# Kernel tuning notes

Hardware: AMD Instinct MI355X
Metric: run time of the kernel (lower is better)

## Reference

```python
import jax, jax.numpy as jnp
import numpy as np
import math

EPS_BN1 = 1e-3   # batch_norm1 eps
EPS_BNP = 1e-5   # predictor BN default eps


def conv1d(x, w, b=None, stride=1, padding=0, dilation=1):
    # x: (B, Cin, T), w: (Cout, Cin, K)
    out = jax.lax.conv_general_dilated(
        x, w, window_strides=(stride,), padding=[(padding, padding)],
        rhs_dilation=(dilation,), dimension_numbers=('NCH', 'OIH', 'NCH'))
    if b is not None:
        out = out + b[None, :, None]
    return out


def bn_eval(x, g, b, m, v, eps):
    scale = g / jnp.sqrt(v + eps)
    return (x - m[None, :, None]) * scale[None, :, None] + b[None, :, None]


def setup_inputs() -> dict:
    key = jax.random.key(0)
    ks = jax.random.split(key, 16)
    B, Cin, T = 16, 256, 4096
    Cout, P = 256, 32
    f32 = jnp.float32

    def n(k, shape, s):
        return s * jax.random.normal(k, shape, dtype=f32)

    inp = {
        'x': n(ks[0], (B, Cin, T), 1.0),
        'conv1_w': n(ks[1], (2 * Cout, Cin, 1), 0.06),
        'bn1_g': 1.0 + n(ks[2], (2 * Cout,), 0.1),
        'bn1_b': n(ks[3], (2 * Cout,), 0.1),
        'bn1_m': n(ks[4], (2 * Cout,), 0.1),
        'bn1_v': 1.0 + 0.1 * jax.random.uniform(ks[5], (2 * Cout,), dtype=f32),
        'conv1x1_w': n(ks[6], (1, Cin, 1), 0.06),
        'p0_w': n(ks[7], (P, 2, 31), 0.1),
        'p0_b': n(ks[8], (P,), 0.05),
        'p0bn_g': jnp.ones((P,), f32), 'p0bn_b': jnp.zeros((P,), f32),
        'p0bn_m': n(ks[9], (P,), 0.1),
        'p0bn_v': 1.0 + 0.1 * jax.random.uniform(ks[10], (P,), dtype=f32),
        'p1_w': n(ks[11], (P, P, 15), 0.05),
        'p1_b': n(ks[12], (P,), 0.05),
        'p1bn_g': jnp.ones((P,), f32), 'p1bn_b': jnp.zeros((P,), f32),
        'p1bn_m': n(ks[13], (P,), 0.1),
        'p1bn_v': 1.0 + 0.1 * jax.random.uniform(ks[14], (P,), dtype=f32),
        # last predictor conv: weight scaled by 0.01, bias = -log(2) (per __init__)
        'p2_w': 0.01 * n(ks[15], (2, P, 15), 0.05),
        'p2_b': jnp.array([-math.log(2.0), -math.log(2.0)], dtype=f32),
        'norm_mean': jnp.ones((1,), f32),  # registered buffer, eval renorm
    }
    return inp


def _forward(x, conv1_w, bn1_g, bn1_b, bn1_m, bn1_v, conv1x1_w,
             p0_w, p0_b, p0bn_g, p0bn_b, p0bn_m, p0bn_v,
             p1_w, p1_b, p1bn_g, p1bn_b, p1bn_m, p1bn_v,
             p2_w, p2_b, norm_mean):
    B, Cin, T = x.shape
    sg = jax.lax.stop_gradient

    # conv1 -> BN -> GLU(dim=1); dropout is identity in eval
    feat = bn_eval(conv1d(x, conv1_w), bn1_g, bn1_b, bn1_m, bn1_v, EPS_BN1)
    a, g = jnp.split(feat, 2, axis=1)
    feat = a * jax.nn.sigmoid(g)                     # (B, Cout, T)

    # predictor on [__x, __x^2]
    xx = conv1d(x, conv1x1_w)                        # (B, 1, T)
    h = jnp.concatenate([xx, xx * xx], axis=1)       # (B, 2, T)
    h = jax.nn.silu(bn_eval(conv1d(h, p0_w, p0_b, padding=15),
                            p0bn_g, p0bn_b, p0bn_m, p0bn_v, EPS_BNP))
    h = jax.nn.silu(bn_eval(conv1d(h, p1_w, p1_b, padding=7),
                            p1bn_g, p1bn_b, p1bn_m, p1bn_v, EPS_BNP))
    jumps = conv1d(h, p2_w, p2_b, padding=7)         # (B, 2, T)

    weights = jax.nn.sigmoid(jumps[:, 0, :])         # (B, T)
    moves = jax.nn.sigmoid(jumps[:, 1, :]) * norm_mean[0]  # eval: renorm = norm_mean
    row_renorm = jnp.maximum(jnp.mean(moves, axis=1), 1.0)
    moves = moves / row_renorm[:, None]

    features = jnp.transpose(feat, (0, 2, 1))        # (B, T, C)
    fw = features * weights[:, :, None]

    # big_pool: poses value = cumsum(moves); grad path = local window of 21 moves
    # (the k=1..20 shift loop adds grad-only terms). Window sum via cumsum diff.
    c = jnp.cumsum(moves, axis=1)
    win = c - jnp.pad(c, ((0, 0), (21, 0)))[:, :T]   # sum of moves[i-20..i]
    poses = sg(c) + win - sg(win)                    # (B, T)

    floors = jnp.floor(poses)
    ceils = floors + 1.0
    w1 = 1.0 - (poses - floors)                      # func = line: 1 - t
    w2 = 1.0 - (ceils - poses)

    # moves <= 1 (sigmoid * norm_mean=1 / row_renorm>=1) => ceils.max()+1 <= T+2
    L = T + 2                                        # static bound for out length
    C = features.shape[2]
    bidx = jnp.arange(B)[:, None]
    fi = floors.astype(jnp.int32)
    ci = fi + 1
    out = jnp.zeros((B, L, C), dtype=features.dtype)
    out = out.at[bidx, fi].add(w1[:, :, None] * fw)
    out = out.at[bidx, ci].add(w2[:, :, None] * fw)

    x_evs = jnp.transpose(out, (0, 2, 1))            # (B, C, L)
    pad = 15 - (L % 15)                              # F.pad(0, 15 - L % 15)
    return jnp.pad(x_evs, ((0, 0), (0, 0), (0, pad)))


def reference(x, conv1_w, bn1_g, bn1_b, bn1_m, bn1_v, conv1x1_w,
              p0_w, p0_b, p0bn_g, p0bn_b, p0bn_m, p0bn_v,
              p1_w, p1_b, p1bn_g, p1bn_b, p1bn_m, p1bn_v,
              p2_w, p2_b, norm_mean):
    return _forward(x, conv1_w, bn1_g, bn1_b, bn1_m, bn1_v, conv1x1_w,
                    p0_w, p0_b, p0bn_g, p0bn_b, p0bn_m, p0bn_v,
                    p1_w, p1_b, p1bn_g, p1bn_b, p1bn_m, p1bn_v,
                    p2_w, p2_b, norm_mean)
```

## Files before the change

kernel.cpp:

```cpp
#include <hip/hip_runtime.h>
#include <hip/hip_bf16.h>

#define BB   16
#define CIN  256
#define TN   4096
#define LOUT 4110
#define FTS  4224

typedef __attribute__((ext_vector_type(8))) short s16x8;
typedef __attribute__((ext_vector_type(4))) float f32x4;


__global__ __launch_bounds__(256) void k0_prep(
    const float* __restrict__ conv1_w, const float* __restrict__ p0_w,
    const float* __restrict__ p1_w, const float* __restrict__ p2_w,
    const float* __restrict__ bn1_g, const float* __restrict__ bn1_b,
    const float* __restrict__ bn1_m, const float* __restrict__ bn1_v,
    const float* __restrict__ p0_b, const float* __restrict__ p0g,
    const float* __restrict__ p0bb, const float* __restrict__ p0m,
    const float* __restrict__ p0v,
    const float* __restrict__ p1_b, const float* __restrict__ p1g,
    const float* __restrict__ p1bb, const float* __restrict__ p1m,
    const float* __restrict__ p1v,
    short* __restrict__ wBpk, float4* __restrict__ bnp,
    float* __restrict__ wp0T, short* __restrict__ wp1M,
    short* __restrict__ wp2M, float2* __restrict__ bnp0,
    float2* __restrict__ bnp1) {
  int bid = blockIdx.x, tid = threadIdx.x;
  if (bid < 512) {
    int e = bid * 256 + tid;
    int i = e & 7, l = (e >> 3) & 63, ks = (e >> 9) & 7, n16 = e >> 12;
    int n = n16 * 16 + (l & 15);
    int j = n & 63;
    int co = (j < 32) ? ((n >> 6) * 32 + j) : (256 + (n >> 6) * 32 + (j - 32));
    int ci = ks * 32 + (l >> 4) * 8 + i;
    __hip_bfloat16 hv = __float2bfloat16(conv1_w[co * 256 + ci]);
    wBpk[e] = *(short*)&hv;
  } else {
    int idx = (bid - 512) * 256 + tid;
    if (idx < 1984) {
      int ch = idx & 31, rem = idx >> 5;
      int ic = rem / 31, k = rem % 31;
      wp0T[idx] = p0_w[(ch * 2 + ic) * 31 + k];
    }
    {
      int i = idx & 7, l = (idx >> 3) & 63, nf = (idx >> 9) & 1, koff = idx >> 10;
      int ch = nf * 16 + (l & 15), ic = (l >> 4) * 8 + i;
      __hip_bfloat16 hv = __float2bfloat16(p1_w[(ch * 32 + ic) * 15 + koff]);
      wp1M[idx] = *(short*)&hv;
    }
    if (idx < 7680) {
      int i = idx & 7, l = (idx >> 3) & 63, koff = idx >> 9;
      int n = l & 15, ic = (l >> 4) * 8 + i;
      float v = (n < 2) ? p2_w[(n * 32 + ic) * 15 + koff] : 0.f;
      __hip_bfloat16 hv = __float2bfloat16(v);
      wp2M[idx] = *(short*)&hv;
    }
    if (idx < 32) {
      int ch = idx;
      float sc = p0g[ch] * rsqrtf(p0v[ch] + 1e-5f);
      bnp0[ch] = make_float2(sc, (p0_b[ch] - p0m[ch]) * sc + p0bb[ch]);
    }
    if (idx >= 32 && idx < 64) {
      int ch = idx - 32;
      float sc = p1g[ch] * rsqrtf(p1v[ch] + 1e-5f);
      bnp1[ch] = make_float2(sc, (p1_b[ch] - p1m[ch]) * sc + p1bb[ch]);
    }
    if (idx < 256) {
      int c = idx;
      float sa = bn1_g[c] * rsqrtf(bn1_v[c] + 1e-3f);
      float ba = bn1_b[c] - bn1_m[c] * sa;
      float sg = bn1_g[c + 256] * rsqrtf(bn1_v[c + 256] + 1e-3f);
      float bg = bn1_b[c + 256] - bn1_m[c + 256] * sg;
      bnp[c] = make_float4(sa, ba, sg, bg);
    }
  }
}

__global__ __launch_bounds__(256) void k0b_tr(
    const float* __restrict__ x, const float* __restrict__ w1x1,
    short* __restrict__ xT, float* __restrict__ xx) {
  int t0 = blockIdx.x * 64;
  int b = blockIdx.y;
  __shared__ float ls[64][129];
  int tid = threadIdx.x;
  const float* xb = x + (size_t)b * (CIN * TN);
  float xacc = 0.f;
  for (int half = 0; half < 2; ++half) {
    if (half) __syncthreads();
#pragma unroll
    for (int s = 0; s < 8; ++s) {
      int idx = tid + s * 256;
      int ci = idx >> 4, tc = idx & 15;
      float4 v = *(const float4*)(xb + (size_t)(half * 128 + ci) * TN + t0 + tc * 4);
      ls[tc * 4 + 0][ci] = v.x;
      ls[tc * 4 + 1][ci] = v.y;
      ls[tc * 4 + 2][ci] = v.z;
      ls[tc * 4 + 3][ci] = v.w;
    }
    __syncthreads();
    if (tid < 64) {
#pragma unroll 4
      for (int k = 0; k < 128; ++k)
        xacc = fmaf(ls[tid][k], w1x1[half * 128 + k], xacc);
    }
#pragma unroll
    for (int s = 0; s < 4; ++s) {
      int o = tid + s * 256;
      int ci8 = o & 15, t = o >> 4;
      s16x8 pk;
#pragma unroll
      for (int i = 0; i < 8; ++i) {
        __hip_bfloat16 hv = __float2bfloat16(ls[t][ci8 * 8 + i]);
        pk[i] = *(short*)&hv;
      }
      *(s16x8*)(xT + ((size_t)(b * TN) + t0 + t) * 256 + half * 128 + ci8 * 8) = pk;
    }
  }
  if (tid < 64) xx[b * TN + t0 + tid] = xacc;
}

__global__ __launch_bounds__(512) void k1_mfma(
    const short* __restrict__ xT, const short* __restrict__ wBpk,
    const float4* __restrict__ bnp, __hip_bfloat16* __restrict__ featT) {
  int ty = blockIdx.x, b = blockIdx.y;
  int t0 = ty * 64;
  __shared__ __align__(16) short As[64 * 256];
  int tid = threadIdx.x;
  int l = tid & 63, wv = tid >> 6;
  const short* xb = xT + ((size_t)b * TN + t0) * 256;

#pragma unroll
  for (int it = 0; it < 4; ++it) {
    int r = it * 16 + wv * 2 + (l >> 5);
    int gs = (l & 31) ^ (r & 7);
    const short* gp = xb + r * 256 + gs * 8;
    __builtin_amdgcn_global_load_lds(
        (const __attribute__((address_space(1))) void*)gp,
        (__attribute__((address_space(3))) void*)(As + (it * 16 + wv * 2) * 256),
        16, 0, 0);
  }
  __syncthreads();

  f32x4 acc[4][4];
#pragma unroll
  for (int i = 0; i < 4; ++i)
#pragma unroll
    for (int j = 0; j < 4; ++j) acc[i][j] = (f32x4){0.f, 0.f, 0.f, 0.f};

  int lr = l & 15, lk = l >> 4;
  const short* wrow = wBpk + (size_t)l * 8;

#pragma unroll 2
  for (int ks = 0; ks < 8; ++ks) {
    s16x8 bf[4], af[4];
#pragma unroll
    for (int nf = 0; nf < 4; ++nf)
      bf[nf] = *(const s16x8*)(wrow + (size_t)(wv * 4 + nf) * 4096 + ks * 512);
#pragma unroll
    for (int mf = 0; mf < 4; ++mf) {
      int r = mf * 16 + lr;
      int phys = (ks * 4 + lk) ^ (r & 7);
      af[mf] = *(const s16x8*)(As + r * 256 + phys * 8);
    }
#pragma unroll
    for (int mf = 0; mf < 4; ++mf)
#pragma unroll
      for (int nf = 0; nf < 4; ++nf)
        acc[mf][nf] = __builtin_amdgcn_mfma_f32_16x16x32_bf16(
            af[mf], bf[nf], acc[mf][nf], 0, 0, 0);
  }

  int cb = wv * 32;
#pragma unroll
  for (int nf = 0; nf < 2; ++nf) {
    float4 bn = bnp[cb + nf * 16 + lr];
    int c = cb + nf * 16 + lr;
#pragma unroll
    for (int mf = 0; mf < 4; ++mf) {
#pragma unroll
      for (int r = 0; r < 4; ++r) {
        float a = acc[mf][nf][r], g = acc[mf][nf + 2][r];
        float av = fmaf(a, bn.x, bn.y);
        float gv = fmaf(g, bn.z, bn.w);
        float fv = av / (1.f + __expf(-gv));
        int t = t0 + mf * 16 + lk * 4 + r;
        featT[((size_t)b * TN + t) * 256 + c] = __float2bfloat16(fv);
      }
    }
  }
}

__global__ __launch_bounds__(512) void k2_pred(
    const float* __restrict__ xx,
    const float* __restrict__ wp0T, const float2* __restrict__ bnp0,
    const short* __restrict__ wp1M, const float2* __restrict__ bnp1,
    const short* __restrict__ wp2M, const float* __restrict__ p2_b,
    const float* __restrict__ norm_mean,
    float* __restrict__ wts, float* __restrict__ mvr) {
  int t0 = blockIdx.x * 128;
  int b = blockIdx.y;
  __shared__ float xin[2][192];
  __shared__ short h0T[160 * 40];
  __shared__ short h1T[144 * 40];
  int tid = threadIdx.x;
  for (int q = tid; q < 192; q += 512) {
    int t = t0 - 29 + q;
    float v = (q < 186 && t >= 0 && t < TN) ? xx[b * TN + t] : 0.f;
    xin[0][q] = v;
    xin[1][q] = v * v;
  }
  __syncthreads();
  {
    int ch = tid & 31, tq = tid >> 5;
    int i0 = tq * 12;
    if (i0 < 156) {
      float2 bb0 = bnp0[ch];
      float a0[12];
#pragma unroll
      for (int j = 0; j < 12; ++j) a0[j] = 0.f;
#pragma unroll
      for (int ic = 0; ic < 2; ++ic) {
        float rr[44];
#pragma unroll
        for (int q = 0; q < 11; ++q) {
          float4 t4 = *(const float4*)(&xin[ic][i0 + q * 4]);
          rr[q * 4 + 0] = t4.x; rr[q * 4 + 1] = t4.y;
          rr[q * 4 + 2] = t4.z; rr[q * 4 + 3] = t4.w;
        }
#pragma unroll
        for (int k = 0; k < 31; ++k) {
          float w = wp0T[(ic * 31 + k) * 32 + ch];
#pragma unroll
          for (int j = 0; j < 12; ++j) a0[j] = fmaf(w, rr[j + k], a0[j]);
        }
      }
#pragma unroll
      for (int j = 0; j < 12; ++j) {
        int i = i0 + j;
        if (i < 156) {
          float v = a0[j] * bb0.x + bb0.y;
          float h = v / (1.f + __expf(-v));
          __hip_bfloat16 hv = __float2bfloat16(h);
          h0T[i * 40 + ch] = *(short*)&hv;
        }
      }
    }
    if (tid < 128) h0T[(156 + (tid >> 5)) * 40 + (tid & 31)] = 0;
  }
  __syncthreads();
  int l = tid & 63, wv = tid >> 6;
  int lrow = l & 15, lk8 = (l >> 4) * 8;
  {
    f32x4 acc[2][2];
#pragma unroll
    for (int i = 0; i < 2; ++i)
#pragma unroll
      for (int j = 0; j < 2; ++j) acc[i][j] = (f32x4){0.f, 0.f, 0.f, 0.f};
    int nmf = (wv == 0) ? 2 : 1;
    for (int koff = 0; koff < 15; ++koff) {
      const short* bp = wp1M + koff * 1024;
      s16x8 bf0 = *(const s16x8*)(bp + l * 8);
      s16x8 bf1 = *(const s16x8*)(bp + 512 + l * 8);
      for (int mi = 0; mi < nmf; ++mi) {
        int mf = (mi == 0) ? wv : 8;
        s16x8 af = *(const s16x8*)(&h0T[(mf * 16 + koff + lrow) * 40 + lk8]);
        acc[mi][0] = __builtin_amdgcn_mfma_f32_16x16x32_bf16(af, bf0, acc[mi][0], 0, 0, 0);
        acc[mi][1] = __builtin_amdgcn_mfma_f32_16x16x32_bf16(af, bf1, acc[mi][1], 0, 0, 0);
      }
    }
    for (int mi = 0; mi < nmf; ++mi) {
      int mf = (mi == 0) ? wv : 8;
#pragma unroll
      for (int nf = 0; nf < 2; ++nf) {
        int ch = nf * 16 + lrow;
        float2 bb = bnp1[ch];
#pragma unroll
        for (int r = 0; r < 4; ++r) {
          int row = mf * 16 + (l >> 4) * 4 + r;
          float v = acc[mi][nf][r] * bb.x + bb.y;
          float h = v / (1.f + __expf(-v));
          __hip_bfloat16 hv = __float2bfloat16(h);
          h1T[row * 40 + ch] = *(short*)&hv;
        }
      }
    }
  }
  __syncthreads();
  {
    f32x4 acc2 = (f32x4){0.f, 0.f, 0.f, 0.f};
    for (int koff = 0; koff < 15; ++koff) {
      s16x8 bf = *(const s16x8*)(wp2M + koff * 512 + l * 8);
      s16x8 af = *(const s16x8*)(&h1T[(wv * 16 + koff + lrow) * 40 + lk8]);
      acc2 = __builtin_amdgcn_mfma_f32_16x16x32_bf16(af, bf, acc2, 0, 0, 0);
    }
    int ch = lrow;
    if (ch < 2) {
      float pb = p2_b[ch];
      float nm = norm_mean[0];
#pragma unroll
      for (int r = 0; r < 4; ++r) {
        int t = t0 + wv * 16 + (l >> 4) * 4 + r;
        float a = acc2[r] + pb;
        float s = 1.f / (1.f + __expf(-a));
        if (ch == 0) wts[b * TN + t] = s;
        else         mvr[b * TN + t] = s * nm;
      }
    }
  }
}

__global__ __launch_bounds__(256) void k3_scan(const float* __restrict__ mvr,
                                               float* __restrict__ poses,
                                               int* __restrict__ firstT) {
  int b = blockIdx.x, tid = threadIdx.x;
  __shared__ float csum[256];
  __shared__ int shlast;
  float v[16];
  const float* src = mvr + b * TN + tid * 16;
  float run = 0.f;
#pragma unroll
  for (int j = 0; j < 16; ++j) { run += src[j]; v[j] = run; }
  csum[tid] = run;
  __syncthreads();
  for (int off = 1; off < 256; off <<= 1) {
    float tv = (tid >= off) ? csum[tid - off] : 0.f;
    __syncthreads();
    csum[tid] += tv;
    __syncthreads();
  }
  float incl = csum[tid];
  float total = csum[255];
  float excl = incl - run;
  __syncthreads();
  float rn = total * (1.0f / 4096.0f);
  float inv = (rn > 1.0f) ? 1.0f / rn : 1.0f;
  float p16[16];
  float* pd = poses + b * TN + tid * 16;
#pragma unroll
  for (int j = 0; j < 16; ++j) { p16[j] = (excl + v[j]) * inv; pd[j] = p16[j]; }
  csum[tid] = p16[15];
  __syncthreads();
  int* ft = firstT + b * FTS;
  int prevf = (tid == 0) ? -1 : min((int)floorf(csum[tid - 1]), 4220);
  int f = prevf;
#pragma unroll
  for (int j = 0; j < 16; ++j) {
    f = min((int)floorf(p16[j]), 4220);
    for (int l = prevf + 1; l <= f; ++l) ft[l] = tid * 16 + j;
    prevf = f;
  }
  if (tid == 255) shlast = f;
  __syncthreads();
  for (int l = shlast + 1 + tid; l < FTS; l += 256) ft[l] = TN;
}

__global__ __launch_bounds__(256) void k4_gather(
    const __hip_bfloat16* __restrict__ featT, const float* __restrict__ wts,
    const float* __restrict__ poses, const int* __restrict__ firstT,
    float* __restrict__ out) {
  int d = blockIdx.x + 257 * blockIdx.y;
  int w = (d & 7) * 514 + (d >> 3);
  int lx = w % 257, b = w / 257;
  int l0 = lx * 16;
  __shared__ float acc[16][259];
  int tid = threadIdx.x;
  for (int i = tid; i < 16 * 259; i += 256) ((float*)acc)[i] = 0.f;
  const int* ft = firstT + b * FTS;
  int ts = (l0 == 0) ? 0 : ft[l0 - 1];
  int te = ft[l0 + 16];
  __syncthreads();
  int c = tid;
  if (ts < te) {
    const float* pp = poses + b * TN;
    const float* wp = wts + b * TN;
    const __hip_bfloat16* fp = featT + (size_t)(b * TN) * 256 + c;
    float p_cur = pp[ts];
    float w_cur = wp[ts];
    float f_cur = __bfloat162float(fp[(size_t)ts * 256]);
    float S_lo = 0.f, S_hi = 0.f;
    int cur = (int)floorf(p_cur);
    for (int t = ts; t < te; ++t) {
      float p_nxt = 0.f, w_nxt = 0.f, f_nxt = 0.f;
      if (t + 1 < te) {
        p_nxt = pp[t + 1];
        w_nxt = wp[t + 1];
        f_nxt = __bfloat162float(fp[(size_t)(t + 1) * 256]);
      }
      int fi = (int)floorf(p_cur);
      if (fi < cur) fi = cur;
      if (fi != cur) {
        int r = cur - l0;
        if (r >= 0 && r < 16) acc[r][c] = S_lo;
        if (fi == cur + 1) {
          S_lo = S_hi;
        } else {
          int r2 = cur + 1 - l0;
          if (r2 >= 0 && r2 < 16) acc[r2][c] = S_hi;
          S_lo = 0.f;
        }
        S_hi = 0.f;
        cur = fi;
      }
      float w2 = p_cur - (float)fi;
      float fw = f_cur * w_cur;
      S_lo = fmaf(1.f - w2, fw, S_lo);
      S_hi = fmaf(w2, fw, S_hi);
      p_cur = p_nxt; w_cur = w_nxt; f_cur = f_nxt;
    }
    int r = cur - l0;
    if (r >= 0 && r < 16) acc[r][c] = S_lo;
    int r2 = cur + 1 - l0;
    if (r2 >= 0 && r2 < 16) acc[r2][c] = S_hi;
  }
  __syncthreads();
  for (int i = tid; i < 4096; i += 256) {
    int c2 = i >> 4, r = i & 15;
    int l = l0 + r;
    if (l < LOUT) out[((size_t)b * 256 + c2) * LOUT + l] = acc[r][c2];
  }
}

extern "C" void kernel_launch(void* const* d_in, const int* in_sizes, int n_in,
                              void* d_out, int out_size, void* d_ws, size_t ws_size,
                              hipStream_t stream) {
  const float* x       = (const float*)d_in[0];
  const float* conv1_w = (const float*)d_in[1];
  const float* bn1_g   = (const float*)d_in[2];
  const float* bn1_b   = (const float*)d_in[3];
  const float* bn1_m   = (const float*)d_in[4];
  const float* bn1_v   = (const float*)d_in[5];
  const float* w1x1    = (const float*)d_in[6];
  const float* p0_w    = (const float*)d_in[7];
  const float* p0_b    = (const float*)d_in[8];
  const float* p0g     = (const float*)d_in[9];
  const float* p0bb    = (const float*)d_in[10];
  const float* p0m     = (const float*)d_in[11];
  const float* p0v     = (const float*)d_in[12];
  const float* p1_w    = (const float*)d_in[13];
  const float* p1_b    = (const float*)d_in[14];
  const float* p1g     = (const float*)d_in[15];
  const float* p1bb    = (const float*)d_in[16];
  const float* p1m     = (const float*)d_in[17];
  const float* p1v     = (const float*)d_in[18];
  const float* p2_w    = (const float*)d_in[19];
  const float* p2_b    = (const float*)d_in[20];
  const float* nmean   = (const float*)d_in[21];

  char* ws = (char*)d_ws;
  __hip_bfloat16* featT = (__hip_bfloat16*)ws;
  short* wBpk   = (short*)(ws + 33554432);
  float4* bnp   = (float4*)(ws + 33816576);
  float* wp0T   = (float*)(ws + 33820672);
  short* wp1M   = (short*)(ws + 33828864);
  short* wp2M   = (short*)(ws + 33859584);
  float2* bnp0  = (float2*)(ws + 33874944);
  float2* bnp1  = (float2*)(ws + 33875200);
  float* xx     = (float*)(ws + 33890304);
  float* wts    = (float*)(ws + 34152448);
  float* mvr    = (float*)(ws + 34414592);
  float* poses  = (float*)(ws + 34676736);
  int*   firstT = (int*)  (ws + 34938880);
  float* out    = (float*)d_out;
  short* xT     = (short*)d_out;

  k0_prep<<<dim3(572), dim3(256), 0, stream>>>(
      conv1_w, p0_w, p1_w, p2_w, bn1_g, bn1_b, bn1_m, bn1_v,
      p0_b, p0g, p0bb, p0m, p0v, p1_b, p1g, p1bb, p1m, p1v,
      wBpk, bnp, wp0T, wp1M, wp2M, bnp0, bnp1);
  k0b_tr<<<dim3(64, 16), dim3(256), 0, stream>>>(x, w1x1, xT, xx);
  k1_mfma<<<dim3(64, 16), dim3(512), 0, stream>>>(xT, wBpk, bnp, featT);
  k2_pred<<<dim3(32, 16), dim3(512), 0, stream>>>(xx, wp0T, bnp0, wp1M, bnp1,
                                                  wp2M, p2_b, nmean, wts, mvr);
  k3_scan<<<dim3(16), dim3(256), 0, stream>>>(mvr, poses, firstT);
  k4_gather<<<dim3(257, 16), dim3(256), 0, stream>>>(featT, wts, poses, firstT, out);
}
```

Measured before the change: 105.9 us.

## Fuse transpose/bf16 conversion and 1x1 reduction into the MFMA GEMM kernel

Removes the separate transpose kernel that wrote a bf16 transposed copy of x to global memory. The GEMM kernel now loads a 64x256 fp32 tile of x into LDS, computes the 1x1 conv reduction with an 8-lane shuffle reduction, and converts fp32 to bf16 on the fly when building MFMA A fragments. This avoids one kernel launch and a full write plus read of the intermediate. In exchange it uses about 64 KB of LDS per block, which limits occupancy, and it repeats scalar bf16 conversions inside the MFMA loop.

```diff
diff --git a/kernel.cpp b/kernel.cpp
--- a/kernel.cpp
+++ b/kernel.cpp
@@ -77,77 +77,46 @@
   }
 }
 
-__global__ __launch_bounds__(256) void k0b_tr(
+__global__ __launch_bounds__(512, 4) void k1_mfma(
     const float* __restrict__ x, const float* __restrict__ w1x1,
-    short* __restrict__ xT, float* __restrict__ xx) {
-  int t0 = blockIdx.x * 64;
-  int b = blockIdx.y;
-  __shared__ float ls[64][129];
+    const short* __restrict__ wBpk, const float4* __restrict__ bnp,
+    __hip_bfloat16* __restrict__ featT, float* __restrict__ xx) {
+  int ty = blockIdx.x, b = blockIdx.y;
+  int t0 = ty * 64;
+  __shared__ float ls[64][257];
   int tid = threadIdx.x;
   const float* xb = x + (size_t)b * (CIN * TN);
-  float xacc = 0.f;
-  for (int half = 0; half < 2; ++half) {
-    if (half) __syncthreads();
-#pragma unroll
-    for (int s = 0; s < 8; ++s) {
-      int idx = tid + s * 256;
-      int ci = idx >> 4, tc = idx & 15;
-      float4 v = *(const float4*)(xb + (size_t)(half * 128 + ci) * TN + t0 + tc * 4);
-      ls[tc * 4 + 0][ci] = v.x;
-      ls[tc * 4 + 1][ci] = v.y;
-      ls[tc * 4 + 2][ci] = v.z;
-      ls[tc * 4 + 3][ci] = v.w;
-    }
-    __syncthreads();
-    if (tid < 64) {
-#pragma unroll 4
-      for (int k = 0; k < 128; ++k)
-        xacc = fmaf(ls[tid][k], w1x1[half * 128 + k], xacc);
-    }
-#pragma unroll
-    for (int s = 0; s < 4; ++s) {
-      int o = tid + s * 256;
-      int ci8 = o & 15, t = o >> 4;
-      s16x8 pk;
-#pragma unroll
-      for (int i = 0; i < 8; ++i) {
-        __hip_bfloat16 hv = __float2bfloat16(ls[t][ci8 * 8 + i]);
-        pk[i] = *(short*)&hv;
-      }
-      *(s16x8*)(xT + ((size_t)(b * TN) + t0 + t) * 256 + half * 128 + ci8 * 8) = pk;
-    }
-  }
-  if (tid < 64) xx[b * TN + t0 + tid] = xacc;
-}
-
-__global__ __launch_bounds__(512) void k1_mfma(
-    const short* __restrict__ xT, const short* __restrict__ wBpk,
-    const float4* __restrict__ bnp, __hip_bfloat16* __restrict__ featT) {
-  int ty = blockIdx.x, b = blockIdx.y;
-  int t0 = ty * 64;
-  __shared__ __align__(16) short As[64 * 256];
-  int tid = threadIdx.x;
+#pragma unroll
+  for (int s = 0; s < 8; ++s) {
+    int idx = tid + s * 512;
+    int ci = idx >> 4, tc = idx & 15;
+    float4 v = *(const float4*)(xb + (size_t)ci * TN + t0 + tc * 4);
+    ls[tc * 4 + 0][ci] = v.x;
+    ls[tc * 4 + 1][ci] = v.y;
+    ls[tc * 4 + 2][ci] = v.z;
+    ls[tc * 4 + 3][ci] = v.w;
+  }
+  __syncthreads();
+
+  {
+    int t = tid >> 3, kq = tid & 7;
+    float a = 0.f;
+#pragma unroll 8
+    for (int j = 0; j < 32; ++j)
+      a = fmaf(ls[t][kq + j * 8], w1x1[kq + j * 8], a);
+    a += __shfl_xor(a, 1);
+    a += __shfl_xor(a, 2);
+    a += __shfl_xor(a, 4);
+    if (kq == 0) xx[b * TN + t0 + t] = a;
+  }
+
+  f32x4 acc[4][4];
+#pragma unroll
+  for (int i = 0; i < 4; ++i)
+#pragma unroll
+    for (int j = 0; j < 4; ++j) acc[i][j] = (f32x4){0.f, 0.f, 0.f, 0.f};
+
   int l = tid & 63, wv = tid >> 6;
-  const short* xb = xT + ((size_t)b * TN + t0) * 256;
-
-#pragma unroll
-  for (int it = 0; it < 4; ++it) {
-    int r = it * 16 + wv * 2 + (l >> 5);
-    int gs = (l & 31) ^ (r & 7);
-    const short* gp = xb + r * 256 + gs * 8;
-    __builtin_amdgcn_global_load_lds(
-        (const __attribute__((address_space(1))) void*)gp,
-        (__attribute__((address_space(3))) void*)(As + (it * 16 + wv * 2) * 256),
-        16, 0, 0);
-  }
-  __syncthreads();
-
-  f32x4 acc[4][4];
-#pragma unroll
-  for (int i = 0; i < 4; ++i)
-#pragma unroll
-    for (int j = 0; j < 4; ++j) acc[i][j] = (f32x4){0.f, 0.f, 0.f, 0.f};
-
   int lr = l & 15, lk = l >> 4;
   const short* wrow = wBpk + (size_t)l * 8;
 
@@ -159,9 +128,14 @@
       bf[nf] = *(const s16x8*)(wrow + (size_t)(wv * 4 + nf) * 4096 + ks * 512);
 #pragma unroll
     for (int mf = 0; mf < 4; ++mf) {
-      int r = mf * 16 + lr;
-      int phys = (ks * 4 + lk) ^ (r & 7);
-      af[mf] = *(const s16x8*)(As + r * 256 + phys * 8);
+      const float* ap = &ls[mf * 16 + lr][ks * 32 + lk * 8];
+      s16x8 t;
+#pragma unroll
+      for (int i = 0; i < 8; ++i) {
+        __hip_bfloat16 hv = __float2bfloat16(ap[i]);
+        t[i] = *(short*)&hv;
+      }
+      af[mf] = t;
     }
 #pragma unroll
     for (int mf = 0; mf < 4; ++mf)
@@ -462,14 +436,12 @@
   float* poses  = (float*)(ws + 34676736);
   int*   firstT = (int*)  (ws + 34938880);
   float* out    = (float*)d_out;
-  short* xT     = (short*)d_out;
 
   k0_prep<<<dim3(572), dim3(256), 0, stream>>>(
       conv1_w, p0_w, p1_w, p2_w, bn1_g, bn1_b, bn1_m, bn1_v,
       p0_b, p0g, p0bb, p0m, p0v, p1_b, p1g, p1bb, p1m, p1v,
       wBpk, bnp, wp0T, wp1M, wp2M, bnp0, bnp1);
-  k0b_tr<<<dim3(64, 16), dim3(256), 0, stream>>>(x, w1x1, xT, xx);
-  k1_mfma<<<dim3(64, 16), dim3(512), 0, stream>>>(xT, wBpk, bnp, featT);
+  k1_mfma<<<dim3(64, 16), dim3(512), 0, stream>>>(x, w1x1, wBpk, bnp, featT, xx);
   k2_pred<<<dim3(32, 16), dim3(512), 0, stream>>>(xx, wp0T, bnp0, wp1M, bnp1,
                                                   wp2M, p2_b, nmean, wts, mvr);
   k3_scan<<<dim3(16), dim3(256), 0, stream>>>(mvr, poses, firstT);
```

After: 98.49 us. 1.08x faster.
